# Optimization experiments

Measured on AMD Instinct MI355X. Metric: run time of the kernel, lower is better.

Reference implementation:

```python
import jax, jax.numpy as jnp
import numpy as np
from jax import lax

B, C, H, W = 8, 128, 128, 128


def setup_inputs() -> dict:
    key = jax.random.key(0)
    ks = jax.random.split(key, 10)
    s = 0.02
    return {
        "x": jax.random.normal(ks[0], (B, C, H, W), jnp.float32),
        "ln_w": jnp.ones((C,), jnp.float32),
        "ln_b": jnp.zeros((C,), jnp.float32),
        "qkv_w": jax.random.normal(ks[1], (3 * C, C, 1, 1), jnp.float32) * s,
        "qkv_b": jnp.zeros((3 * C,), jnp.float32),
        "dw_w": jax.random.normal(ks[2], (3 * C, 1, 3, 3), jnp.float32) * s,
        "dw_b": jnp.zeros((3 * C,), jnp.float32),
        "proj_w": jax.random.normal(ks[3], (C, C, 1, 1), jnp.float32) * s,
        "proj_b": jnp.zeros((C,), jnp.float32),
        "temp1": jnp.ones((1, 1), jnp.float32),
        "temp2": jnp.ones((1, 1), jnp.float32),
    }


def reference(x, ln_w, ln_b, qkv_w, qkv_b, dw_w, dw_b, proj_w, proj_b, temp1, temp2):
    Cd = x.shape[1]

    def ln(t):  # WithBias LayerNorm over channel dim (unbiased=False var)
        mu = t.mean(axis=1, keepdims=True)
        var = ((t - mu) ** 2).mean(axis=1, keepdims=True)
        return (t - mu) / jnp.sqrt(var + 1e-5) * ln_w[None, :, None, None] + ln_b[None, :, None, None]

    def conv1(t, w, b):  # 1x1 conv
        return jnp.einsum('bchw,oc->bohw', t, w[:, :, 0, 0]) + b[None, :, None, None]

    def dwc(t):  # depthwise 3x3, pad 1
        y = lax.conv_general_dilated(t, dw_w, (1, 1), ((1, 1), (1, 1)),
                                     dimension_numbers=('NCHW', 'OIHW', 'NCHW'),
                                     feature_group_count=t.shape[1])
        return y + dw_b[None, :, None, None]

    def l2n(t):  # F.normalize over last axis, eps=1e-12
        return t / jnp.maximum(jnp.linalg.norm(t, axis=-1, keepdims=True), 1e-12)

    # ---- stage 1: pool over H, attention over W (channel-pooled) ----
    qkv = dwc(conv1(ln(x), qkv_w, qkv_b))
    q1, k1, v1 = qkv[:, :Cd], qkv[:, Cd:2 * Cd], qkv[:, 2 * Cd:]
    q1 = l2n(q1.mean(axis=2)[:, None])           # [B,1,C,W]
    k1 = l2n(k1.max(axis=2)[:, None])            # [B,1,C,W]
    attn1 = jax.nn.softmax(jnp.einsum('bocw,bocv->bowv', q1, k1) * temp1, axis=-1)  # [B,1,W,W]
    out1 = jnp.einsum('bchw,bowv->bchv', v1, attn1)
    out1 = x + conv1(out1, proj_w, proj_b)

    # ---- stage 2: pool over C, attention over H ----
    qkv = dwc(conv1(ln(out1), qkv_w, qkv_b))
    q2, k2, v2 = qkv[:, :Cd], qkv[:, Cd:2 * Cd], qkv[:, 2 * Cd:]
    q2 = l2n(q2.mean(axis=1)[:, None])           # [B,1,H,W]
    k2 = l2n(k2.mean(axis=1)[:, None])           # [B,1,H,W]
    attn2 = jax.nn.softmax(jnp.einsum('bohw,bogw->bohg', q2, k2) * temp2, axis=-1)  # [B,1,H,H]
    out2 = jnp.einsum('bchw,bohg->bcgw', v2, attn2)  # = (v^T @ attn)^T
    out = conv1(out2, proj_w, proj_b) + out1
    return out
```

## Files before the change

kernel.cpp:

```cpp
#include <hip/hip_runtime.h>
#include <hip/hip_bf16.h>

typedef __attribute__((ext_vector_type(8))) short bf16x8;
typedef __attribute__((ext_vector_type(4))) float f32x4;
typedef __attribute__((ext_vector_type(4))) unsigned short us4;
typedef __attribute__((ext_vector_type(4))) unsigned int u32x4;

static constexpr int CC = 128, NN = 16384;
static constexpr int O3 = 384;
static constexpr long long CN  = (long long)CC * NN;
static constexpr long long O3N = (long long)O3 * NN;

__device__ __forceinline__ float wave_sum(float v) {
  for (int o = 32; o; o >>= 1) v += __shfl_xor(v, o);
  return v;
}
__device__ __forceinline__ unsigned pk2bf(float a, float b) {
  __hip_bfloat162 h = __float22bfloat162_rn(make_float2(a, b));
  return *reinterpret_cast<unsigned*>(&h);
}
__device__ __forceinline__ unsigned short f2bf(float f) {
  __hip_bfloat16 h = __float2bfloat16(f);
  return *reinterpret_cast<unsigned short*>(&h);
}
__device__ __forceinline__ float bf2f(unsigned short h) {
  return __uint_as_float((unsigned)h << 16);
}

__global__ __launch_bounds__(64) void k_prep(const float* __restrict__ qkvw,
                                             const float* __restrict__ qkvb,
                                             const float* __restrict__ lnw,
                                             const float* __restrict__ lnb,
                                             const float* __restrict__ projw,
                                             unsigned short* __restrict__ Aq,
                                             unsigned short* __restrict__ Ap,
                                             float* __restrict__ Svec,
                                             float* __restrict__ bias2) {
  int o = blockIdx.x, t = threadIdx.x;
  if (o < O3) {
    float w0 = qkvw[o * 128 + t], w1 = qkvw[o * 128 + t + 64];
    unsigned short h0 = f2bf(w0 * lnw[t]), h1 = f2bf(w1 * lnw[t + 64]);
    Aq[o * 128 + t] = h0; Aq[o * 128 + t + 64] = h1;
    float s = wave_sum(bf2f(h0) + bf2f(h1));
    float bs = wave_sum(w0 * lnb[t] + w1 * lnb[t + 64]);
    if (t == 0) { Svec[o] = s; bias2[o] = qkvb[o] + bs; }
  } else {
    int r = o - O3;
    Ap[r * 128 + t] = f2bf(projw[r * 128 + t]);
    Ap[r * 128 + t + 64] = f2bf(projw[r * 128 + t + 64]);
  }
}

__global__ __launch_bounds__(256) void k_qkv_mfma(
    const void* __restrict__ srcp, const float* __restrict__ mu, const float* __restrict__ rs,
    const unsigned short* __restrict__ Aq, const float* __restrict__ Svec,
    const float* __restrict__ bias2, unsigned short* __restrict__ out,
    int b0, int useg, int srcbf) {
  __shared__ unsigned short As[128 * 136];
  __shared__ unsigned short Bs[64 * 128];
  __shared__ float muL[64], rsL[64];
  int bz = blockIdx.z, bg = b0 + bz;
  int p = blockIdx.x;
  int hi = p / 24, rr0 = p - hi * 24;
  int m0 = (rr0 >> 3) * 128;
  int n0 = (hi * 8 + (rr0 & 7)) * 64;
  int t = threadIdx.x, w = t >> 6, l = t & 63;
  int lr = l & 15, lg = l >> 4;

  {
    const unsigned short* Asrc = Aq + (size_t)m0 * 128;
#pragma unroll
    for (int r = 0; r < 8; ++r) {
      int v = r * 256 + t;
      int m = v >> 4, c8 = (v & 15) * 8;
      *(u32x4*)&As[m * 136 + c8] = *(const u32x4*)&Asrc[m * 128 + c8];
    }
  }
  {
    int pg = t & 15, cbk = t >> 4;
    int c8 = cbk * 8;
    if (!srcbf) {
      const float* xb = (const float*)srcp + (size_t)bg * CN + n0 + pg * 4;
      float4 v[8];
#pragma unroll
      for (int ch = 0; ch < 8; ++ch)
        v[ch] = *(const float4*)&xb[(size_t)(c8 + ch) * NN];
#pragma unroll
      for (int pp = 0; pp < 4; ++pp) {
        unsigned pk[4];
#pragma unroll
        for (int q = 0; q < 4; ++q)
          pk[q] = pk2bf(((const float*)&v[2 * q])[pp], ((const float*)&v[2 * q + 1])[pp]);
        int n = pg * 4 + pp;
        *(u32x4*)&Bs[n * 128 + (c8 ^ ((n & 7) << 3))] = *(const u32x4*)pk;
      }
    } else {
      const unsigned short* xb = (const unsigned short*)srcp + (size_t)bg * CN + n0 + pg * 4;
      us4 v[8];
#pragma unroll
      for (int ch = 0; ch < 8; ++ch)
        v[ch] = *(const us4*)&xb[(size_t)(c8 + ch) * NN];
#pragma unroll
      for (int pp = 0; pp < 4; ++pp) {
        unsigned pk[4];
#pragma unroll
        for (int q = 0; q < 4; ++q)
          pk[q] = (unsigned)v[2 * q][pp] | ((unsigned)v[2 * q + 1][pp] << 16);
        int n = pg * 4 + pp;
        *(u32x4*)&Bs[n * 128 + (c8 ^ ((n & 7) << 3))] = *(const u32x4*)pk;
      }
    }
  }
  __syncthreads();

  if (!useg) {
    int pp = t >> 2, sub = t & 3;
    float s1 = 0.f, s2 = 0.f;
#pragma unroll
    for (int b2 = 0; b2 < 4; ++b2) {
      int c8 = (sub * 4 + b2) * 8;
      int c8s = c8 ^ ((pp & 7) << 3);
      bf16x8 v = *(const bf16x8*)&Bs[pp * 128 + c8s];
#pragma unroll
      for (int q = 0; q < 8; ++q) {
        float f = bf2f((unsigned short)v[q]);
        s1 += f; s2 += f * f;
      }
    }
    s1 += __shfl_xor(s1, 1); s2 += __shfl_xor(s2, 1);
    s1 += __shfl_xor(s1, 2); s2 += __shfl_xor(s2, 2);
    if (sub == 0) {
      float m = s1 * (1.f / 128.f);
      muL[pp] = m;
      rsL[pp] = rsqrtf(s2 * (1.f / 128.f) - m * m + 1e-5f);
    }
  }

  f32x4 acc[2][4];
#pragma unroll
  for (int i = 0; i < 2; ++i)
#pragma unroll
    for (int j = 0; j < 4; ++j) acc[i][j] = (f32x4){0.f, 0.f, 0.f, 0.f};
#pragma unroll
  for (int ks = 0; ks < 4; ++ks) {
    bf16x8 bfr[4];
#pragma unroll
    for (int j = 0; j < 4; ++j) {
      int row = 16 * j + lr;
      int col = (ks * 32 + lg * 8) ^ ((lr & 7) << 3);
      bfr[j] = *(const bf16x8*)&Bs[row * 128 + col];
    }
#pragma unroll
    for (int i = 0; i < 2; ++i) {
      bf16x8 afr = *(const bf16x8*)&As[(32 * w + 16 * i + lr) * 136 + ks * 32 + lg * 8];
#pragma unroll
      for (int j = 0; j < 4; ++j)
        acc[i][j] = __builtin_amdgcn_mfma_f32_16x16x32_bf16(afr, bfr[j], acc[i][j], 0, 0, 0);
    }
  }
  __syncthreads();

  float rsv[4], muv[4];
#pragma unroll
  for (int j = 0; j < 4; ++j) {
    int nl = 16 * j + lr;
    if (useg) {
      rsv[j] = rs[(size_t)bg * NN + n0 + nl];
      muv[j] = mu[(size_t)bg * NN + n0 + nl];
    } else {
      rsv[j] = rsL[nl];
      muv[j] = muL[nl];
    }
  }
  unsigned short* Os = As;
#pragma unroll
  for (int i = 0; i < 2; ++i) {
    int obl = 32 * w + 16 * i + lg * 4;
    float sv[4], bv[4];
#pragma unroll
    for (int r2 = 0; r2 < 4; ++r2) { sv[r2] = Svec[m0 + obl + r2]; bv[r2] = bias2[m0 + obl + r2]; }
#pragma unroll
    for (int j = 0; j < 4; ++j) {
      float rm = rsv[j] * muv[j];
#pragma unroll
      for (int r2 = 0; r2 < 4; ++r2)
        Os[(obl + r2) * 72 + 16 * j + lr] =
            f2bf(fmaf(rsv[j], acc[i][j][r2], bv[r2] - rm * sv[r2]));
    }
  }
  __syncthreads();
#pragma unroll
  for (int r = 0; r < 4; ++r) {
    int idx = r * 256 + t;
    int row = idx >> 3, ch = idx & 7;
    unsigned short* op = out + (size_t)bz * O3N + (size_t)(m0 + row) * NN + n0 + ch * 8;
    *(u32x4*)op = *(const u32x4*)&Os[row * 72 + ch * 8];
  }
}

__global__ __launch_bounds__(1024) void k_dwc(unsigned short* __restrict__ buf,
                                              const float* __restrict__ dww,
                                              const float* __restrict__ dwb,
                                              float* __restrict__ qm,
                                              float* __restrict__ km,
                                              int b0, int stage) {
  __shared__ unsigned short pl[130 * 144];
  __shared__ float red[32 * 128];
  int o = blockIdx.x, bz = blockIdx.y, bg = b0 + bz;
  int t = threadIdx.x;
  unsigned short* base = buf + (size_t)bz * O3N + (size_t)o * NN;
  unsigned* pl32 = (unsigned*)pl;

  for (int i = t; i < 1168; i += 1024) {
    int idx;
    if (i < 72) idx = i;
    else if (i < 144) idx = 129 * 72 + (i - 72);
    else { int j = i - 144; int row = (j >> 3) + 1; int s = j & 7;
           idx = row * 72 + (s < 4 ? s : 64 + s); }
    pl32[idx] = 0u;
  }
  __syncthreads();
#pragma unroll
  for (int r = 0; r < 2; ++r) {
    int idx = r * 1024 + t;
    int row = idx >> 4, c8 = (idx & 15) * 8;
    *(u32x4*)&pl[(row + 1) * 144 + 8 + c8] = *(const u32x4*)&base[row * 128 + c8];
  }
  __syncthreads();

  const float* wg = dww + o * 9;
  float w00 = wg[0], w01 = wg[1], w02 = wg[2];
  float w10 = wg[3], w11 = wg[4], w12 = wg[5];
  float w20 = wg[6], w21 = wg[7], w22 = wg[8];
  float bias = dwb[o];
  int mode = (stage == 0) ? (o < 128 ? 1 : (o < 256 ? 2 : 0)) : 0;
  int hh0 = t >> 5, w0 = (t & 31) * 4;
  float csum[4] = {0.f, 0.f, 0.f, 0.f};
  float cmax[4] = {-1e30f, -1e30f, -1e30f, -1e30f};

#pragma unroll
  for (int g = 0; g < 4; ++g) {
    int h = g * 32 + hh0;
    float a0 = bias, a1 = bias, a2 = bias, a3 = bias;
#pragma unroll
    for (int dr = 0; dr < 3; ++dr) {
      const unsigned short* rp = &pl[(h + dr) * 144];
      us4 cA = *(const us4*)&rp[w0 + 4];
      us4 cB = *(const us4*)&rp[w0 + 8];
      us4 cC = *(const us4*)&rp[w0 + 12];
      float f0 = bf2f(cA[3]), f1 = bf2f(cB[0]), f2 = bf2f(cB[1]);
      float f3 = bf2f(cB[2]), f4 = bf2f(cB[3]), f5 = bf2f(cC[0]);
      float wr0 = (dr == 0) ? w00 : (dr == 1 ? w10 : w20);
      float wr1 = (dr == 0) ? w01 : (dr == 1 ? w11 : w21);
      float wr2 = (dr == 0) ? w02 : (dr == 1 ? w12 : w22);
      a0 += f0 * wr0 + f1 * wr1 + f2 * wr2;
      a1 += f1 * wr0 + f2 * wr1 + f3 * wr2;
      a2 += f2 * wr0 + f3 * wr1 + f4 * wr2;
      a3 += f3 * wr0 + f4 * wr1 + f5 * wr2;
    }
    if (mode == 0) {
      unsigned lo = pk2bf(a0, a1), hi2 = pk2bf(a2, a3);
      uint2 ov = make_uint2(lo, hi2);
      *(uint2*)&base[g * 4096 + t * 4] = ov;
    } else if (mode == 1) {
      csum[0] += a0; csum[1] += a1; csum[2] += a2; csum[3] += a3;
    } else {
      cmax[0] = fmaxf(cmax[0], a0); cmax[1] = fmaxf(cmax[1], a1);
      cmax[2] = fmaxf(cmax[2], a2); cmax[3] = fmaxf(cmax[3], a3);
    }
  }

  if (mode) {
    int j = t >> 5;
#pragma unroll
    for (int dx = 0; dx < 4; ++dx)
      red[j * 128 + w0 + dx] = (mode == 1) ? csum[dx] : cmax[dx];
    __syncthreads();
    if (t < 128) {
      float v = red[t];
      if (mode == 1) {
        for (int jj = 1; jj < 32; ++jj) v += red[jj * 128 + t];
        qm[(size_t)bg * NN + o * 128 + t] = v * (1.f / 128.f);
      } else {
        for (int jj = 1; jj < 32; ++jj) v = fmaxf(v, red[jj * 128 + t]);
        km[(size_t)bg * NN + (o - 128) * 128 + t] = v;
      }
    }
  }
}

__global__ __launch_bounds__(256) void k_reduce2(const unsigned short* __restrict__ qkv,
                                                 float* __restrict__ qm, float* __restrict__ km,
                                                 int b0) {
  int bz = blockIdx.y;
  int n = blockIdx.x * 256 + threadIdx.x;
  const unsigned short* base = qkv + (size_t)bz * O3N + n;
  float sq = 0.f, sk = 0.f;
#pragma unroll 4
  for (int c = 0; c < 128; ++c) {
    sq += bf2f(base[(size_t)c * NN]);
    sk += bf2f(base[(size_t)(c + 128) * NN]);
  }
  size_t off = (size_t)(b0 + bz) * NN + n;
  qm[off] = sq * (1.f / 128.f);
  km[off] = sk * (1.f / 128.f);
}

__global__ void k_norm2(float* __restrict__ qm, float* __restrict__ km, int row0) {
  float* buf = blockIdx.y ? km : qm;
  int r = row0 + blockIdx.x, t = threadIdx.x;
  float* p = buf + (size_t)r * 128;
  float v0 = p[t], v1 = p[t + 64];
  float s = wave_sum(v0 * v0 + v1 * v1);
  float sc = 1.f / fmaxf(sqrtf(s), 1e-12f);
  p[t] = v0 * sc;
  p[t + 64] = v1 * sc;
}

__global__ void k_attn1(const float* __restrict__ qm, const float* __restrict__ km,
                        const float* __restrict__ temp, unsigned short* __restrict__ attnT,
                        int b0) {
  int bg = b0 + blockIdx.y;
  int i = blockIdx.x, t = threadIdx.x;
  const float* qb = qm + (size_t)bg * NN;
  const float* kb = km + (size_t)bg * NN;
  __shared__ float qcol[128];
  __shared__ float wred[2];
  float mxw, smw;
  qcol[t] = qb[t * 128 + i];
  __syncthreads();
  float s = 0.f;
#pragma unroll 4
  for (int k = 0; k < 128; ++k) s += qcol[k] * kb[k * 128 + t];
  s *= temp[0];
  int wid = t >> 6, lane = t & 63;
  mxw = s;
  for (int o = 32; o; o >>= 1) mxw = fmaxf(mxw, __shfl_xor(mxw, o));
  if (lane == 0) wred[wid] = mxw;
  __syncthreads();
  float mx = fmaxf(wred[0], wred[1]);
  float pv = __expf(s - mx);
  __syncthreads();
  smw = wave_sum(pv);
  if (lane == 0) wred[wid] = smw;
  __syncthreads();
  float denom = wred[0] + wred[1];
  attnT[(size_t)bg * NN + (size_t)t * 128 + i] = f2bf(pv / denom);
}

__global__ void k_attn2(const float* __restrict__ qm, const float* __restrict__ km,
                        const float* __restrict__ temp, unsigned short* __restrict__ attnT,
                        int b0) {
  int bg = b0 + blockIdx.y;
  int i = blockIdx.x, t = threadIdx.x;
  const float* qb = qm + (size_t)bg * NN + i * 128;
  const float* kb = km + (size_t)bg * NN + (size_t)t * 128;
  __shared__ float qrow[128];
  __shared__ float wred[2];
  qrow[t] = qb[t];
  __syncthreads();
  float s = 0.f;
#pragma unroll 4
  for (int w = 0; w < 128; ++w) s += qrow[w] * kb[w];
  s *= temp[0];
  int wid = t >> 6, lane = t & 63;
  float mxw = s;
  for (int o = 32; o; o >>= 1) mxw = fmaxf(mxw, __shfl_xor(mxw, o));
  if (lane == 0) wred[wid] = mxw;
  __syncthreads();
  float mx = fmaxf(wred[0], wred[1]);
  float pv = __expf(s - mx);
  __syncthreads();
  float smw = wave_sum(pv);
  if (lane == 0) wred[wid] = smw;
  __syncthreads();
  float denom = wred[0] + wred[1];
  attnT[(size_t)bg * NN + (size_t)t * 128 + i] = f2bf(pv / denom);
}

__global__ __launch_bounds__(256) void k_ap1(const unsigned short* __restrict__ buf,
                                             const unsigned short* __restrict__ attnT,
                                             const unsigned short* __restrict__ Ap,
                                             const float* __restrict__ pb,
                                             const float* __restrict__ x,
                                             unsigned short* __restrict__ out1,
                                             float* __restrict__ mu, float* __restrict__ rs,
                                             int b0) {
  __shared__ __attribute__((aligned(16))) unsigned short S[32768];
  unsigned short* TA = S;
  unsigned short* TB = S + 16384;
  int h = blockIdx.x, bz = blockIdx.z, bg = b0 + bz;
  int t = threadIdx.x, wv = t >> 6, l = t & 63, lr = l & 15, lg = l >> 4;

  {
    const unsigned short* vbase = buf + (size_t)bz * O3N + (size_t)256 * NN;
    const unsigned short* abase = attnT + (size_t)bg * NN;
#pragma unroll
    for (int r = 0; r < 8; ++r) {
      int idx = r * 256 + t;
      int row = idx >> 4, c8 = (idx & 15) * 8;
      int c8s = c8 ^ ((row & 7) << 3);
      *(u32x4*)&TA[row * 128 + c8s] = *(const u32x4*)&vbase[((size_t)row * 128 + h) * 128 + c8];
      *(u32x4*)&TB[row * 128 + c8s] = *(const u32x4*)&abase[row * 128 + c8];
    }
  }
  __syncthreads();

  f32x4 acc[2][8];
#pragma unroll
  for (int i = 0; i < 2; ++i)
#pragma unroll
    for (int j = 0; j < 8; ++j) acc[i][j] = (f32x4){0.f, 0.f, 0.f, 0.f};
#pragma unroll
  for (int ks = 0; ks < 4; ++ks) {
    int colx = (ks * 32 + lg * 8) ^ ((lr & 7) << 3);
    bf16x8 bfr[8];
#pragma unroll
    for (int j = 0; j < 8; ++j)
      bfr[j] = *(const bf16x8*)&TB[(16 * j + lr) * 128 + colx];
#pragma unroll
    for (int i = 0; i < 2; ++i) {
      bf16x8 afr = *(const bf16x8*)&TA[(32 * wv + 16 * i + lr) * 128 + colx];
#pragma unroll
      for (int j = 0; j < 8; ++j)
        acc[i][j] = __builtin_amdgcn_mfma_f32_16x16x32_bf16(afr, bfr[j], acc[i][j], 0, 0, 0);
    }
  }
  __syncthreads();

#pragma unroll
  for (int i = 0; i < 2; ++i) {
    int c0 = 32 * wv + 16 * i + lg * 4;
#pragma unroll
    for (int j = 0; j < 8; ++j) {
      int v = 16 * j + lr;
      uint2 ov = make_uint2(pk2bf(acc[i][j][0], acc[i][j][1]),
                            pk2bf(acc[i][j][2], acc[i][j][3]));
      *(uint2*)&TA[v * 128 + (c0 ^ ((v & 7) << 3))] = ov;
    }
  }
#pragma unroll
  for (int r = 0; r < 8; ++r) {
    int idx = r * 256 + t;
    int row = idx >> 4, c8 = (idx & 15) * 8;
    *(u32x4*)&TB[row * 128 + (c8 ^ ((row & 7) << 3))] = *(const u32x4*)&Ap[row * 128 + c8];
  }
  __syncthreads();

#pragma unroll
  for (int i = 0; i < 2; ++i)
#pragma unroll
    for (int j = 0; j < 8; ++j) acc[i][j] = (f32x4){0.f, 0.f, 0.f, 0.f};
#pragma unroll
  for (int ks = 0; ks < 4; ++ks) {
    int colx = (ks * 32 + lg * 8) ^ ((lr & 7) << 3);
    bf16x8 bfr[8];
#pragma unroll
    for (int j = 0; j < 8; ++j)
      bfr[j] = *(const bf16x8*)&TA[(16 * j + lr) * 128 + colx];
#pragma unroll
    for (int i = 0; i < 2; ++i) {
      bf16x8 afr = *(const bf16x8*)&TB[(32 * wv + 16 * i + lr) * 128 + colx];
#pragma unroll
      for (int j = 0; j < 8; ++j)
        acc[i][j] = __builtin_amdgcn_mfma_f32_16x16x32_bf16(afr, bfr[j], acc[i][j], 0, 0, 0);
    }
  }
  __syncthreads();

  unsigned short* Os = S;
  float* red1 = (float*)(S + 17408);
  float* red2 = red1 + 128 * 17;
  float s1p[8], s2p[8];
#pragma unroll
  for (int j = 0; j < 8; ++j) { s1p[j] = 0.f; s2p[j] = 0.f; }
#pragma unroll
  for (int i = 0; i < 2; ++i) {
    int o0 = 32 * wv + 16 * i + lg * 4;
    float bv[4];
#pragma unroll
    for (int r2 = 0; r2 < 4; ++r2) bv[r2] = pb[o0 + r2];
#pragma unroll
    for (int j = 0; j < 8; ++j) {
      int n = h * 128 + 16 * j + lr;
#pragma unroll
      for (int r2 = 0; r2 < 4; ++r2) {
        size_t off = (size_t)bg * CN + (size_t)(o0 + r2) * NN + n;
        float val = acc[i][j][r2] + bv[r2] + x[off];
        Os[(o0 + r2) * 136 + 16 * j + lr] = f2bf(val);
        s1p[j] += val;
        s2p[j] += val * val;
      }
    }
  }
#pragma unroll
  for (int j = 0; j < 8; ++j) {
    red1[(16 * j + lr) * 17 + (wv * 4 + lg)] = s1p[j];
    red2[(16 * j + lr) * 17 + (wv * 4 + lg)] = s2p[j];
  }
  __syncthreads();
#pragma unroll
  for (int r = 0; r < 8; ++r) {
    int idx = r * 256 + t;
    int row = idx >> 4, ch = idx & 15;
    unsigned short* op = out1 + (size_t)bg * CN + (size_t)row * NN + h * 128 + ch * 8;
    *(u32x4*)op = *(const u32x4*)&Os[row * 136 + ch * 8];
  }
  if (t < 128) {
    float s1 = 0.f, s2 = 0.f;
#pragma unroll
    for (int kk = 0; kk < 16; ++kk) { s1 += red1[t * 17 + kk]; s2 += red2[t * 17 + kk]; }
    float m = s1 * (1.f / 128.f);
    float var = s2 * (1.f / 128.f) - m * m;
    mu[(size_t)bg * NN + h * 128 + t] = m;
    rs[(size_t)bg * NN + h * 128 + t] = rsqrtf(var + 1e-5f);
  }
}

__global__ __launch_bounds__(256) void k_apply2_mfma(unsigned short* __restrict__ buf,
                                                     const unsigned short* __restrict__ attnT,
                                                     int b0) {
  __shared__ unsigned short At[128 * 136];
  __shared__ unsigned short Bt[128 * 136];
  int bz = blockIdx.z, bg = b0 + bz, c = blockIdx.x;
  int t = threadIdx.x, w = t >> 6, l = t & 63, lr = l & 15, lg = l >> 4;
  const unsigned short* vsrc = buf + (size_t)bz * O3N + (size_t)(256 + c) * NN;
  const unsigned short* asrc = attnT + (size_t)bg * NN;
#pragma unroll
  for (int r = 0; r < 8; ++r) {
    int idx = r * 256 + t;
    int row = idx >> 4, c8 = (idx & 15) * 8;
    *(u32x4*)&At[row * 136 + c8] = *(const u32x4*)&asrc[row * 128 + c8];
    us4 lo = *(const us4*)&vsrc[row * 128 + c8];
    us4 hi = *(const us4*)&vsrc[row * 128 + c8 + 4];
#pragma unroll
    for (int q = 0; q < 4; ++q) {
      Bt[(c8 + q) * 136 + row] = lo[q];
      Bt[(c8 + 4 + q) * 136 + row] = hi[q];
    }
  }
  __syncthreads();
  f32x4 acc[2][8];
#pragma unroll
  for (int i = 0; i < 2; ++i)
#pragma unroll
    for (int j = 0; j < 8; ++j) acc[i][j] = (f32x4){0.f, 0.f, 0.f, 0.f};
#pragma unroll
  for (int ks = 0; ks < 4; ++ks) {
    bf16x8 bfr[8];
#pragma unroll
    for (int j = 0; j < 8; ++j)
      bfr[j] = *(const bf16x8*)&Bt[(16 * j + lr) * 136 + ks * 32 + lg * 8];
#pragma unroll
    for (int i = 0; i < 2; ++i) {
      bf16x8 afr = *(const bf16x8*)&At[(32 * w + 16 * i + lr) * 136 + ks * 32 + lg * 8];
#pragma unroll
      for (int j = 0; j < 8; ++j)
        acc[i][j] = __builtin_amdgcn_mfma_f32_16x16x32_bf16(afr, bfr[j], acc[i][j], 0, 0, 0);
    }
  }
  __syncthreads();
  unsigned short* Os = At;
#pragma unroll
  for (int i = 0; i < 2; ++i)
#pragma unroll
    for (int j = 0; j < 8; ++j) {
      int g = 32 * w + 16 * i + lg * 4;
      Os[g * 136 + 16 * j + lr + 0 * 136] = f2bf(acc[i][j][0]);
      Os[(g + 1) * 136 + 16 * j + lr] = f2bf(acc[i][j][1]);
      Os[(g + 2) * 136 + 16 * j + lr] = f2bf(acc[i][j][2]);
      Os[(g + 3) * 136 + 16 * j + lr] = f2bf(acc[i][j][3]);
    }
  __syncthreads();
  unsigned short* ob = buf + (size_t)bz * O3N + (size_t)c * NN;
#pragma unroll
  for (int r = 0; r < 8; ++r) {
    int idx = r * 256 + t;
    int row = idx >> 4, ch = idx & 15;
    *(u32x4*)&ob[(size_t)row * 128 + ch * 8] = *(const u32x4*)&Os[row * 136 + ch * 8];
  }
}

__global__ __launch_bounds__(256) void k_proj_mfma(
    const unsigned short* __restrict__ tin, const unsigned short* __restrict__ Ap,
    const float* __restrict__ pb, const unsigned short* __restrict__ res,
    float* __restrict__ dst, int b0) {
  __shared__ unsigned short Al[128 * 136];
  __shared__ unsigned short Bs2[64 * 128];
  int bz = blockIdx.z, bg = b0 + bz;
  int n0 = blockIdx.x * 64;
  int t = threadIdx.x, w = t >> 6, l = t & 63, lr = l & 15, lg = l >> 4;

#pragma unroll
  for (int r = 0; r < 8; ++r) {
    int v = r * 256 + t;
    int m = v >> 4, c8 = (v & 15) * 8;
    *(u32x4*)&Al[m * 136 + c8] = *(const u32x4*)&Ap[m * 128 + c8];
  }
  {
    int pg = t & 15, cbk = t >> 4;
    int c8 = cbk * 8;
    const unsigned short* tb = tin + (size_t)bz * O3N + n0 + pg * 4;
    us4 v[8];
#pragma unroll
    for (int ch = 0; ch < 8; ++ch)
      v[ch] = *(const us4*)&tb[(size_t)(c8 + ch) * NN];
#pragma unroll
    for (int pp = 0; pp < 4; ++pp) {
      unsigned pk[4];
#pragma unroll
      for (int q = 0; q < 4; ++q)
        pk[q] = (unsigned)v[2 * q][pp] | ((unsigned)v[2 * q + 1][pp] << 16);
      int n = pg * 4 + pp;
      *(u32x4*)&Bs2[n * 128 + (c8 ^ ((n & 7) << 3))] = *(const u32x4*)pk;
    }
  }
  __syncthreads();

  f32x4 acc[2][4];
#pragma unroll
  for (int i = 0; i < 2; ++i)
#pragma unroll
    for (int j = 0; j < 4; ++j) acc[i][j] = (f32x4){0.f, 0.f, 0.f, 0.f};

#pragma unroll
  for (int ks = 0; ks < 4; ++ks) {
    bf16x8 bfr[4];
#pragma unroll
    for (int j = 0; j < 4; ++j) {
      int row = 16 * j + lr;
      int col = (ks * 32 + lg * 8) ^ ((lr & 7) << 3);
      bfr[j] = *(const bf16x8*)&Bs2[row * 128 + col];
    }
#pragma unroll
    for (int i = 0; i < 2; ++i) {
      bf16x8 afr = *(const bf16x8*)&Al[(32 * w + 16 * i + lr) * 136 + ks * 32 + lg * 8];
#pragma unroll
      for (int j = 0; j < 4; ++j)
        acc[i][j] = __builtin_amdgcn_mfma_f32_16x16x32_bf16(afr, bfr[j], acc[i][j], 0, 0, 0);
    }
  }

#pragma unroll
  for (int i = 0; i < 2; ++i) {
    int ob = 32 * w + 16 * i + lg * 4;
    float bv[4];
#pragma unroll
    for (int r2 = 0; r2 < 4; ++r2) bv[r2] = pb[ob + r2];
#pragma unroll
    for (int j = 0; j < 4; ++j) {
      int n = n0 + 16 * j + lr;
#pragma unroll
      for (int r2 = 0; r2 < 4; ++r2) {
        size_t off = (size_t)bg * CN + (size_t)(ob + r2) * NN + n;
        dst[off] = acc[i][j][r2] + bv[r2] + bf2f(res[off]);
      }
    }
  }
}

extern "C" void kernel_launch(void* const* d_in, const int* in_sizes, int n_in,
                              void* d_out, int out_size, void* d_ws, size_t ws_size,
                              hipStream_t stream) {
  (void)in_sizes; (void)n_in; (void)out_size;
  const float* x     = (const float*)d_in[0];
  const float* lnw   = (const float*)d_in[1];
  const float* lnb   = (const float*)d_in[2];
  const float* qkvw  = (const float*)d_in[3];
  const float* qkvb  = (const float*)d_in[4];
  const float* dww   = (const float*)d_in[5];
  const float* dwb   = (const float*)d_in[6];
  const float* projw = (const float*)d_in[7];
  const float* projb = (const float*)d_in[8];
  const float* temp1 = (const float*)d_in[9];
  const float* temp2 = (const float*)d_in[10];
  float* out = (float*)d_out;
  float* ws = (float*)d_ws;

  auto needBytes = [&](int nb) {
    return ((size_t)nb * (O3N / 2) + 4ull * CN + 4ull * 131072 + 65536 + 768 + 24576 + 8192) * 4;
  };
  int NB = 8;
  while (NB > 1 && ws_size < needBytes(NB)) NB >>= 1;
  if (ws_size < needBytes(1)) return;

  unsigned short* convbuf = (unsigned short*)ws;
  unsigned short* out1 = (unsigned short*)(ws + (size_t)NB * (O3N / 2));
  float* mu = ws + (size_t)NB * (O3N / 2) + 4ull * CN;
  float* rs = mu + 131072;
  float* qm = rs + 131072;
  float* km = qm + 131072;
  unsigned short* attnT = (unsigned short*)(km + 131072);
  float* Svec  = (float*)(attnT + 8ull * NN);
  float* bias2 = Svec + 384;
  unsigned short* Aq = (unsigned short*)(bias2 + 384);
  unsigned short* Ap = Aq + 49152;

  k_prep<<<512, 64, 0, stream>>>(qkvw, qkvb, lnw, lnb, projw, Aq, Ap, Svec, bias2);

  for (int b0 = 0; b0 < 8; b0 += NB) {
    k_qkv_mfma<<<dim3(768, 1, NB), 256, 0, stream>>>(x, mu, rs, Aq, Svec, bias2, convbuf,
                                                     b0, 0, 0);
    k_dwc<<<dim3(384, NB), 1024, 0, stream>>>(convbuf, dww, dwb, qm, km, b0, 0);
    k_norm2<<<dim3(NB * 128, 2), 64, 0, stream>>>(qm, km, b0 * 128);
    k_attn1<<<dim3(128, NB), 128, 0, stream>>>(qm, km, temp1, attnT, b0);
    k_ap1<<<dim3(128, 1, NB), 256, 0, stream>>>(convbuf, attnT, Ap, projb, x, out1, mu, rs, b0);
  }
  for (int b0 = 0; b0 < 8; b0 += NB) {
    k_qkv_mfma<<<dim3(768, 1, NB), 256, 0, stream>>>(out1, mu, rs, Aq, Svec, bias2, convbuf,
                                                     b0, 1, 1);
    k_dwc<<<dim3(384, NB), 1024, 0, stream>>>(convbuf, dww, dwb, qm, km, b0, 1);
    k_reduce2<<<dim3(64, NB), 256, 0, stream>>>(convbuf, qm, km, b0);
    k_norm2<<<dim3(NB * 128, 2), 64, 0, stream>>>(qm, km, b0 * 128);
    k_attn2<<<dim3(128, NB), 128, 0, stream>>>(qm, km, temp2, attnT, b0);
    k_apply2_mfma<<<dim3(128, 1, NB), 256, 0, stream>>>(convbuf, attnT, b0);
    k_proj_mfma<<<dim3(256, 1, NB), 256, 0, stream>>>(convbuf, Ap, projb, out1, out, b0);
  }
}
```

Before: 276.8 us.

## Write qkv GEMM output in tiled layout and split conv buffers

The qkv GEMM now writes each 128x64 output tile as one contiguous block in a separate tiled buffer (convT), so each block's store is a single contiguous region instead of 128 strided rows. The depthwise conv reads from this tiled layout and writes its planar result to a second buffer (convP), which downstream kernels consume. The B-operand shared-memory tiles are also padded from 128 to 136 columns to change bank mapping. The cost is twice the conv workspace, which may lower the batch chunk size NB when the workspace is small, and dwc reads are now gathered across tiles.

Result: slower. 322.5 us (+16.5%).

```diff
diff --git a/kernel.cpp b/kernel.cpp
--- a/kernel.cpp
+++ b/kernel.cpp
@@ -54,16 +54,17 @@
 __global__ __launch_bounds__(256) void k_qkv_mfma(
     const void* __restrict__ srcp, const float* __restrict__ mu, const float* __restrict__ rs,
     const unsigned short* __restrict__ Aq, const float* __restrict__ Svec,
-    const float* __restrict__ bias2, unsigned short* __restrict__ out,
+    const float* __restrict__ bias2, unsigned short* __restrict__ outT,
     int b0, int useg, int srcbf) {
   __shared__ unsigned short As[128 * 136];
-  __shared__ unsigned short Bs[64 * 128];
+  __shared__ unsigned short Bs[64 * 136];
   __shared__ float muL[64], rsL[64];
   int bz = blockIdx.z, bg = b0 + bz;
   int p = blockIdx.x;
   int hi = p / 24, rr0 = p - hi * 24;
   int m0 = (rr0 >> 3) * 128;
-  int n0 = (hi * 8 + (rr0 & 7)) * 64;
+  int tile = hi * 8 + (rr0 & 7);
+  int n0 = tile * 64;
   int t = threadIdx.x, w = t >> 6, l = t & 63;
   int lr = l & 15, lg = l >> 4;
 
@@ -92,7 +93,7 @@
         for (int q = 0; q < 4; ++q)
           pk[q] = pk2bf(((const float*)&v[2 * q])[pp], ((const float*)&v[2 * q + 1])[pp]);
         int n = pg * 4 + pp;
-        *(u32x4*)&Bs[n * 128 + (c8 ^ ((n & 7) << 3))] = *(const u32x4*)pk;
+        *(u32x4*)&Bs[n * 136 + (c8 ^ ((n & 7) << 3))] = *(const u32x4*)pk;
       }
     } else {
       const unsigned short* xb = (const unsigned short*)srcp + (size_t)bg * CN + n0 + pg * 4;
@@ -107,7 +108,7 @@
         for (int q = 0; q < 4; ++q)
           pk[q] = (unsigned)v[2 * q][pp] | ((unsigned)v[2 * q + 1][pp] << 16);
         int n = pg * 4 + pp;
-        *(u32x4*)&Bs[n * 128 + (c8 ^ ((n & 7) << 3))] = *(const u32x4*)pk;
+        *(u32x4*)&Bs[n * 136 + (c8 ^ ((n & 7) << 3))] = *(const u32x4*)pk;
       }
     }
   }
@@ -120,7 +121,7 @@
     for (int b2 = 0; b2 < 4; ++b2) {
       int c8 = (sub * 4 + b2) * 8;
       int c8s = c8 ^ ((pp & 7) << 3);
-      bf16x8 v = *(const bf16x8*)&Bs[pp * 128 + c8s];
+      bf16x8 v = *(const bf16x8*)&Bs[pp * 136 + c8s];
 #pragma unroll
       for (int q = 0; q < 8; ++q) {
         float f = bf2f((unsigned short)v[q]);
@@ -148,7 +149,7 @@
     for (int j = 0; j < 4; ++j) {
       int row = 16 * j + lr;
       int col = (ks * 32 + lg * 8) ^ ((lr & 7) << 3);
-      bfr[j] = *(const bf16x8*)&Bs[row * 128 + col];
+      bfr[j] = *(const bf16x8*)&Bs[row * 136 + col];
     }
 #pragma unroll
     for (int i = 0; i < 2; ++i) {
@@ -189,16 +190,17 @@
     }
   }
   __syncthreads();
+  unsigned short* op0 = outT + ((size_t)bz * 256 + tile) * 24576 + (size_t)m0 * 64;
 #pragma unroll
   for (int r = 0; r < 4; ++r) {
     int idx = r * 256 + t;
     int row = idx >> 3, ch = idx & 7;
-    unsigned short* op = out + (size_t)bz * O3N + (size_t)(m0 + row) * NN + n0 + ch * 8;
-    *(u32x4*)op = *(const u32x4*)&Os[row * 72 + ch * 8];
-  }
-}
-
-__global__ __launch_bounds__(1024) void k_dwc(unsigned short* __restrict__ buf,
+    *(u32x4*)&op0[row * 64 + ch * 8] = *(const u32x4*)&Os[row * 72 + ch * 8];
+  }
+}
+
+__global__ __launch_bounds__(1024) void k_dwc(const unsigned short* __restrict__ convT,
+                                              unsigned short* __restrict__ convP,
                                               const float* __restrict__ dww,
                                               const float* __restrict__ dwb,
                                               float* __restrict__ qm,
@@ -208,7 +210,6 @@
   __shared__ float red[32 * 128];
   int o = blockIdx.x, bz = blockIdx.y, bg = b0 + bz;
   int t = threadIdx.x;
-  unsigned short* base = buf + (size_t)bz * O3N + (size_t)o * NN;
   unsigned* pl32 = (unsigned*)pl;
 
   for (int i = t; i < 1168; i += 1024) {
@@ -220,11 +221,15 @@
     pl32[idx] = 0u;
   }
   __syncthreads();
-#pragma unroll
-  for (int r = 0; r < 2; ++r) {
-    int idx = r * 1024 + t;
-    int row = idx >> 4, c8 = (idx & 15) * 8;
-    *(u32x4*)&pl[(row + 1) * 144 + 8 + c8] = *(const u32x4*)&base[row * 128 + c8];
+  {
+    const unsigned short* tb = convT + (size_t)bz * O3N + (size_t)o * 64;
+#pragma unroll
+    for (int r = 0; r < 2; ++r) {
+      int idx = r * 1024 + t;
+      int row = idx >> 4, c8 = (idx & 15) * 8;
+      int tile = (row << 1) | (c8 >> 6), off = c8 & 63;
+      *(u32x4*)&pl[(row + 1) * 144 + 8 + c8] = *(const u32x4*)&tb[(size_t)tile * 24576 + off];
+    }
   }
   __syncthreads();
 
@@ -237,6 +242,7 @@
   int hh0 = t >> 5, w0 = (t & 31) * 4;
   float csum[4] = {0.f, 0.f, 0.f, 0.f};
   float cmax[4] = {-1e30f, -1e30f, -1e30f, -1e30f};
+  unsigned short* base_out = convP + (size_t)bz * O3N + (size_t)o * NN;
 
 #pragma unroll
   for (int g = 0; g < 4; ++g) {
@@ -259,9 +265,8 @@
       a3 += f3 * wr0 + f4 * wr1 + f5 * wr2;
     }
     if (mode == 0) {
-      unsigned lo = pk2bf(a0, a1), hi2 = pk2bf(a2, a3);
-      uint2 ov = make_uint2(lo, hi2);
-      *(uint2*)&base[g * 4096 + t * 4] = ov;
+      uint2 ov = make_uint2(pk2bf(a0, a1), pk2bf(a2, a3));
+      *(uint2*)&base_out[g * 4096 + t * 4] = ov;
     } else if (mode == 1) {
       csum[0] += a0; csum[1] += a1; csum[2] += a2; csum[3] += a3;
     } else {
@@ -326,7 +331,6 @@
   const float* kb = km + (size_t)bg * NN;
   __shared__ float qcol[128];
   __shared__ float wred[2];
-  float mxw, smw;
   qcol[t] = qb[t * 128 + i];
   __syncthreads();
   float s = 0.f;
@@ -334,14 +338,14 @@
   for (int k = 0; k < 128; ++k) s += qcol[k] * kb[k * 128 + t];
   s *= temp[0];
   int wid = t >> 6, lane = t & 63;
-  mxw = s;
+  float mxw = s;
   for (int o = 32; o; o >>= 1) mxw = fmaxf(mxw, __shfl_xor(mxw, o));
   if (lane == 0) wred[wid] = mxw;
   __syncthreads();
   float mx = fmaxf(wred[0], wred[1]);
   float pv = __expf(s - mx);
   __syncthreads();
-  smw = wave_sum(pv);
+  float smw = wave_sum(pv);
   if (lane == 0) wred[wid] = smw;
   __syncthreads();
   float denom = wred[0] + wred[1];
@@ -378,7 +382,7 @@
   attnT[(size_t)bg * NN + (size_t)t * 128 + i] = f2bf(pv / denom);
 }
 
-__global__ __launch_bounds__(256) void k_ap1(const unsigned short* __restrict__ buf,
+__global__ __launch_bounds__(256) void k_ap1(const unsigned short* __restrict__ convP,
                                              const unsigned short* __restrict__ attnT,
                                              const unsigned short* __restrict__ Ap,
                                              const float* __restrict__ pb,
@@ -393,7 +397,7 @@
   int t = threadIdx.x, wv = t >> 6, l = t & 63, lr = l & 15, lg = l >> 4;
 
   {
-    const unsigned short* vbase = buf + (size_t)bz * O3N + (size_t)256 * NN;
+    const unsigned short* vbase = convP + (size_t)bz * O3N + (size_t)256 * NN;
     const unsigned short* abase = attnT + (size_t)bg * NN;
 #pragma unroll
     for (int r = 0; r < 8; ++r) {
@@ -517,14 +521,14 @@
   }
 }
 
-__global__ __launch_bounds__(256) void k_apply2_mfma(unsigned short* __restrict__ buf,
+__global__ __launch_bounds__(256) void k_apply2_mfma(unsigned short* __restrict__ convP,
                                                      const unsigned short* __restrict__ attnT,
                                                      int b0) {
   __shared__ unsigned short At[128 * 136];
   __shared__ unsigned short Bt[128 * 136];
   int bz = blockIdx.z, bg = b0 + bz, c = blockIdx.x;
   int t = threadIdx.x, w = t >> 6, l = t & 63, lr = l & 15, lg = l >> 4;
-  const unsigned short* vsrc = buf + (size_t)bz * O3N + (size_t)(256 + c) * NN;
+  const unsigned short* vsrc = convP + (size_t)bz * O3N + (size_t)(256 + c) * NN;
   const unsigned short* asrc = attnT + (size_t)bg * NN;
 #pragma unroll
   for (int r = 0; r < 8; ++r) {
@@ -566,13 +570,13 @@
 #pragma unroll
     for (int j = 0; j < 8; ++j) {
       int g = 32 * w + 16 * i + lg * 4;
-      Os[g * 136 + 16 * j + lr + 0 * 136] = f2bf(acc[i][j][0]);
+      Os[g * 136 + 16 * j + lr] = f2bf(acc[i][j][0]);
       Os[(g + 1) * 136 + 16 * j + lr] = f2bf(acc[i][j][1]);
       Os[(g + 2) * 136 + 16 * j + lr] = f2bf(acc[i][j][2]);
       Os[(g + 3) * 136 + 16 * j + lr] = f2bf(acc[i][j][3]);
     }
   __syncthreads();
-  unsigned short* ob = buf + (size_t)bz * O3N + (size_t)c * NN;
+  unsigned short* ob = convP + (size_t)bz * O3N + (size_t)c * NN;
 #pragma unroll
   for (int r = 0; r < 8; ++r) {
     int idx = r * 256 + t;
@@ -586,7 +590,7 @@
     const float* __restrict__ pb, const unsigned short* __restrict__ res,
     float* __restrict__ dst, int b0) {
   __shared__ unsigned short Al[128 * 136];
-  __shared__ unsigned short Bs2[64 * 128];
+  __shared__ unsigned short Bs2[64 * 136];
   int bz = blockIdx.z, bg = b0 + bz;
   int n0 = blockIdx.x * 64;
   int t = threadIdx.x, w = t >> 6, l = t & 63, lr = l & 15, lg = l >> 4;
@@ -612,7 +616,7 @@
       for (int q = 0; q < 4; ++q)
         pk[q] = (unsigned)v[2 * q][pp] | ((unsigned)v[2 * q + 1][pp] << 16);
       int n = pg * 4 + pp;
-      *(u32x4*)&Bs2[n * 128 + (c8 ^ ((n & 7) << 3))] = *(const u32x4*)pk;
+      *(u32x4*)&Bs2[n * 136 + (c8 ^ ((n & 7) << 3))] = *(const u32x4*)pk;
     }
   }
   __syncthreads();
@@ -630,7 +634,7 @@
     for (int j = 0; j < 4; ++j) {
       int row = 16 * j + lr;
       int col = (ks * 32 + lg * 8) ^ ((lr & 7) << 3);
-      bfr[j] = *(const bf16x8*)&Bs2[row * 128 + col];
+      bfr[j] = *(const bf16x8*)&Bs2[row * 136 + col];
     }
 #pragma unroll
     for (int i = 0; i < 2; ++i) {
@@ -675,18 +679,19 @@
   const float* temp1 = (const float*)d_in[9];
   const float* temp2 = (const float*)d_in[10];
   float* out = (float*)d_out;
-  float* ws = (float*)d_ws;
-
-  auto needBytes = [&](int nb) {
-    return ((size_t)nb * (O3N / 2) + 4ull * CN + 4ull * 131072 + 65536 + 768 + 24576 + 8192) * 4;
+
+  auto needBytes = [&](size_t nb) {
+    return (2 * nb * (size_t)O3N + 8ull * CN + 8ull * NN + 49152 + 16384) * 2 +
+           (4ull * 131072 + 768) * 4;
   };
-  int NB = 8;
+  size_t NB = 8;
   while (NB > 1 && ws_size < needBytes(NB)) NB >>= 1;
   if (ws_size < needBytes(1)) return;
 
-  unsigned short* convbuf = (unsigned short*)ws;
-  unsigned short* out1 = (unsigned short*)(ws + (size_t)NB * (O3N / 2));
-  float* mu = ws + (size_t)NB * (O3N / 2) + 4ull * CN;
+  unsigned short* convT = (unsigned short*)d_ws;
+  unsigned short* convP = convT + NB * (size_t)O3N;
+  unsigned short* out1  = convP + NB * (size_t)O3N;
+  float* mu = (float*)(out1 + 8ull * CN);
   float* rs = mu + 131072;
   float* qm = rs + 131072;
   float* km = qm + 131072;
@@ -698,22 +703,22 @@
 
   k_prep<<<512, 64, 0, stream>>>(qkvw, qkvb, lnw, lnb, projw, Aq, Ap, Svec, bias2);
 
-  for (int b0 = 0; b0 < 8; b0 += NB) {
-    k_qkv_mfma<<<dim3(768, 1, NB), 256, 0, stream>>>(x, mu, rs, Aq, Svec, bias2, convbuf,
+  for (int b0 = 0; b0 < 8; b0 += (int)NB) {
+    k_qkv_mfma<<<dim3(768, 1, NB), 256, 0, stream>>>(x, mu, rs, Aq, Svec, bias2, convT,
                                                      b0, 0, 0);
-    k_dwc<<<dim3(384, NB), 1024, 0, stream>>>(convbuf, dww, dwb, qm, km, b0, 0);
+    k_dwc<<<dim3(384, NB), 1024, 0, stream>>>(convT, convP, dww, dwb, qm, km, b0, 0);
     k_norm2<<<dim3(NB * 128, 2), 64, 0, stream>>>(qm, km, b0 * 128);
     k_attn1<<<dim3(128, NB), 128, 0, stream>>>(qm, km, temp1, attnT, b0);
-    k_ap1<<<dim3(128, 1, NB), 256, 0, stream>>>(convbuf, attnT, Ap, projb, x, out1, mu, rs, b0);
-  }
-  for (int b0 = 0; b0 < 8; b0 += NB) {
-    k_qkv_mfma<<<dim3(768, 1, NB), 256, 0, stream>>>(out1, mu, rs, Aq, Svec, bias2, convbuf,
+    k_ap1<<<dim3(128, 1, NB), 256, 0, stream>>>(convP, attnT, Ap, projb, x, out1, mu, rs, b0);
+  }
+  for (int b0 = 0; b0 < 8; b0 += (int)NB) {
+    k_qkv_mfma<<<dim3(768, 1, NB), 256, 0, stream>>>(out1, mu, rs, Aq, Svec, bias2, convT,
                                                      b0, 1, 1);
-    k_dwc<<<dim3(384, NB), 1024, 0, stream>>>(convbuf, dww, dwb, qm, km, b0, 1);
-    k_reduce2<<<dim3(64, NB), 256, 0, stream>>>(convbuf, qm, km, b0);
+    k_dwc<<<dim3(384, NB), 1024, 0, stream>>>(convT, convP, dww, dwb, qm, km, b0, 1);
+    k_reduce2<<<dim3(64, NB), 256, 0, stream>>>(convP, qm, km, b0);
     k_norm2<<<dim3(NB * 128, 2), 64, 0, stream>>>(qm, km, b0 * 128);
     k_attn2<<<dim3(128, NB), 128, 0, stream>>>(qm, km, temp2, attnT, b0);
-    k_apply2_mfma<<<dim3(128, 1, NB), 256, 0, stream>>>(convbuf, attnT, b0);
-    k_proj_mfma<<<dim3(256, 1, NB), 256, 0, stream>>>(convbuf, Ap, projb, out1, out, b0);
-  }
-}
+    k_apply2_mfma<<<dim3(128, 1, NB), 256, 0, stream>>>(convP, attnT, b0);
+    k_proj_mfma<<<dim3(256, 1, NB), 256, 0, stream>>>(convP, Ap, projb, out1, out, b0);
+  }
+}
```

## Compute all 384 qkv outputs per block so the input tile is loaded once

Applied to the files above, without the earlier changes.

The qkv 1x1-conv GEMM now has each block cover all 384 output channels for one 64-pixel tile, where before it covered a 128-row slice. The input tile and its LayerNorm statistics are loaded and computed once per tile instead of three times. The weight matrix is streamed through shared memory in 32-wide k-slices with barriers around each. The LDS-staged, vectorized output store is replaced by direct scattered 2-byte global stores, which may hurt write coalescing, and the larger accumulator array raises register pressure.

New measurement: 305.2 us. 1.1x slower.

```diff
diff --git a/kernel.cpp b/kernel.cpp
--- a/kernel.cpp
+++ b/kernel.cpp
@@ -56,26 +56,14 @@
     const unsigned short* __restrict__ Aq, const float* __restrict__ Svec,
     const float* __restrict__ bias2, unsigned short* __restrict__ out,
     int b0, int useg, int srcbf) {
-  __shared__ unsigned short As[128 * 136];
   __shared__ unsigned short Bs[64 * 128];
+  __shared__ unsigned short As[384 * 40];
   __shared__ float muL[64], rsL[64];
   int bz = blockIdx.z, bg = b0 + bz;
-  int p = blockIdx.x;
-  int hi = p / 24, rr0 = p - hi * 24;
-  int m0 = (rr0 >> 3) * 128;
-  int n0 = (hi * 8 + (rr0 & 7)) * 64;
+  int n0 = blockIdx.x * 64;
   int t = threadIdx.x, w = t >> 6, l = t & 63;
   int lr = l & 15, lg = l >> 4;
 
-  {
-    const unsigned short* Asrc = Aq + (size_t)m0 * 128;
-#pragma unroll
-    for (int r = 0; r < 8; ++r) {
-      int v = r * 256 + t;
-      int m = v >> 4, c8 = (v & 15) * 8;
-      *(u32x4*)&As[m * 136 + c8] = *(const u32x4*)&Asrc[m * 128 + c8];
-    }
-  }
   {
     int pg = t & 15, cbk = t >> 4;
     int c8 = cbk * 8;
@@ -136,13 +124,23 @@
     }
   }
 
-  f32x4 acc[2][4];
-#pragma unroll
-  for (int i = 0; i < 2; ++i)
+  f32x4 acc[6][4];
+#pragma unroll
+  for (int i = 0; i < 6; ++i)
 #pragma unroll
     for (int j = 0; j < 4; ++j) acc[i][j] = (f32x4){0.f, 0.f, 0.f, 0.f};
-#pragma unroll
+
+  const unsigned int* Asrc = (const unsigned int*)Aq;
+  unsigned int* Adst = (unsigned int*)As;
   for (int ks = 0; ks < 4; ++ks) {
+    __syncthreads();
+#pragma unroll
+    for (int r = 0; r < 24; ++r) {
+      int idx = r * 256 + t;
+      int o = idx >> 4, cp = idx & 15;
+      Adst[o * 20 + cp] = Asrc[(size_t)o * 64 + ks * 16 + cp];
+    }
+    __syncthreads();
     bf16x8 bfr[4];
 #pragma unroll
     for (int j = 0; j < 4; ++j) {
@@ -151,14 +149,13 @@
       bfr[j] = *(const bf16x8*)&Bs[row * 128 + col];
     }
 #pragma unroll
-    for (int i = 0; i < 2; ++i) {
-      bf16x8 afr = *(const bf16x8*)&As[(32 * w + 16 * i + lr) * 136 + ks * 32 + lg * 8];
+    for (int i = 0; i < 6; ++i) {
+      bf16x8 afr = *(const bf16x8*)&As[(96 * w + 16 * i + lr) * 40 + lg * 8];
 #pragma unroll
       for (int j = 0; j < 4; ++j)
         acc[i][j] = __builtin_amdgcn_mfma_f32_16x16x32_bf16(afr, bfr[j], acc[i][j], 0, 0, 0);
     }
   }
-  __syncthreads();
 
   float rsv[4], muv[4];
 #pragma unroll
@@ -172,29 +169,21 @@
       muv[j] = muL[nl];
     }
   }
-  unsigned short* Os = As;
-#pragma unroll
-  for (int i = 0; i < 2; ++i) {
-    int obl = 32 * w + 16 * i + lg * 4;
+#pragma unroll
+  for (int i = 0; i < 6; ++i) {
+    int ob = 96 * w + 16 * i + lg * 4;
     float sv[4], bv[4];
 #pragma unroll
-    for (int r2 = 0; r2 < 4; ++r2) { sv[r2] = Svec[m0 + obl + r2]; bv[r2] = bias2[m0 + obl + r2]; }
+    for (int r2 = 0; r2 < 4; ++r2) { sv[r2] = Svec[ob + r2]; bv[r2] = bias2[ob + r2]; }
 #pragma unroll
     for (int j = 0; j < 4; ++j) {
+      int n = n0 + 16 * j + lr;
       float rm = rsv[j] * muv[j];
+      unsigned short* op = out + (size_t)bz * O3N + n;
 #pragma unroll
       for (int r2 = 0; r2 < 4; ++r2)
-        Os[(obl + r2) * 72 + 16 * j + lr] =
-            f2bf(fmaf(rsv[j], acc[i][j][r2], bv[r2] - rm * sv[r2]));
-    }
-  }
-  __syncthreads();
-#pragma unroll
-  for (int r = 0; r < 4; ++r) {
-    int idx = r * 256 + t;
-    int row = idx >> 3, ch = idx & 7;
-    unsigned short* op = out + (size_t)bz * O3N + (size_t)(m0 + row) * NN + n0 + ch * 8;
-    *(u32x4*)op = *(const u32x4*)&Os[row * 72 + ch * 8];
+        op[(size_t)(ob + r2) * NN] = f2bf(fmaf(rsv[j], acc[i][j][r2], bv[r2] - rm * sv[r2]));
+    }
   }
 }
 
@@ -259,8 +248,7 @@
       a3 += f3 * wr0 + f4 * wr1 + f5 * wr2;
     }
     if (mode == 0) {
-      unsigned lo = pk2bf(a0, a1), hi2 = pk2bf(a2, a3);
-      uint2 ov = make_uint2(lo, hi2);
+      uint2 ov = make_uint2(pk2bf(a0, a1), pk2bf(a2, a3));
       *(uint2*)&base[g * 4096 + t * 4] = ov;
     } else if (mode == 1) {
       csum[0] += a0; csum[1] += a1; csum[2] += a2; csum[3] += a3;
@@ -326,7 +314,6 @@
   const float* kb = km + (size_t)bg * NN;
   __shared__ float qcol[128];
   __shared__ float wred[2];
-  float mxw, smw;
   qcol[t] = qb[t * 128 + i];
   __syncthreads();
   float s = 0.f;
@@ -334,14 +321,14 @@
   for (int k = 0; k < 128; ++k) s += qcol[k] * kb[k * 128 + t];
   s *= temp[0];
   int wid = t >> 6, lane = t & 63;
-  mxw = s;
+  float mxw = s;
   for (int o = 32; o; o >>= 1) mxw = fmaxf(mxw, __shfl_xor(mxw, o));
   if (lane == 0) wred[wid] = mxw;
   __syncthreads();
   float mx = fmaxf(wred[0], wred[1]);
   float pv = __expf(s - mx);
   __syncthreads();
-  smw = wave_sum(pv);
+  float smw = wave_sum(pv);
   if (lane == 0) wred[wid] = smw;
   __syncthreads();
   float denom = wred[0] + wred[1];
@@ -566,7 +553,7 @@
 #pragma unroll
     for (int j = 0; j < 8; ++j) {
       int g = 32 * w + 16 * i + lg * 4;
-      Os[g * 136 + 16 * j + lr + 0 * 136] = f2bf(acc[i][j][0]);
+      Os[g * 136 + 16 * j + lr] = f2bf(acc[i][j][0]);
       Os[(g + 1) * 136 + 16 * j + lr] = f2bf(acc[i][j][1]);
       Os[(g + 2) * 136 + 16 * j + lr] = f2bf(acc[i][j][2]);
       Os[(g + 3) * 136 + 16 * j + lr] = f2bf(acc[i][j][3]);
@@ -699,7 +686,7 @@
   k_prep<<<512, 64, 0, stream>>>(qkvw, qkvb, lnw, lnb, projw, Aq, Ap, Svec, bias2);
 
   for (int b0 = 0; b0 < 8; b0 += NB) {
-    k_qkv_mfma<<<dim3(768, 1, NB), 256, 0, stream>>>(x, mu, rs, Aq, Svec, bias2, convbuf,
+    k_qkv_mfma<<<dim3(256, 1, NB), 256, 0, stream>>>(x, mu, rs, Aq, Svec, bias2, convbuf,
                                                      b0, 0, 0);
     k_dwc<<<dim3(384, NB), 1024, 0, stream>>>(convbuf, dww, dwb, qm, km, b0, 0);
     k_norm2<<<dim3(NB * 128, 2), 64, 0, stream>>>(qm, km, b0 * 128);
@@ -707,7 +694,7 @@
     k_ap1<<<dim3(128, 1, NB), 256, 0, stream>>>(convbuf, attnT, Ap, projb, x, out1, mu, rs, b0);
   }
   for (int b0 = 0; b0 < 8; b0 += NB) {
-    k_qkv_mfma<<<dim3(768, 1, NB), 256, 0, stream>>>(out1, mu, rs, Aq, Svec, bias2, convbuf,
+    k_qkv_mfma<<<dim3(256, 1, NB), 256, 0, stream>>>(out1, mu, rs, Aq, Svec, bias2, convbuf,
                                                      b0, 1, 1);
     k_dwc<<<dim3(384, NB), 1024, 0, stream>>>(convbuf, dww, dwb, qm, km, b0, 1);
     k_reduce2<<<dim3(64, NB), 256, 0, stream>>>(convbuf, qm, km, b0);
```
